# Performance work log

Hardware: AMD Instinct MI355X
Metric: run time of the kernel (lower is better)

Reference implementation:

```python
import jax, jax.numpy as jnp
import numpy as np

N_NODES = 100000
N_EDGES = 1600000
IN_CH = 128
NHIDDEN = 64
OUT_CH = 40
NLAYERS = 4
ALPHA = 0.1


def setup_inputs() -> dict:
    key = jax.random.key(0)
    ks = jax.random.split(key, 7)
    x = jax.random.normal(ks[0], (N_NODES, IN_CH), dtype=jnp.float32)
    edge_index = jax.random.randint(ks[1], (2, N_EDGES), 0, N_NODES, dtype=jnp.int64)
    batch_graph = jnp.zeros((N_NODES,), dtype=jnp.int64)
    fc1_w = jax.random.normal(ks[2], (NHIDDEN, IN_CH), dtype=jnp.float32) * (1.0 / np.sqrt(IN_CH))
    fc1_b = jax.random.normal(ks[3], (NHIDDEN,), dtype=jnp.float32) * 0.01
    conv_w = jax.random.normal(ks[4], (NLAYERS, NHIDDEN, NHIDDEN), dtype=jnp.float32) * (1.0 / np.sqrt(NHIDDEN))
    fc2_w = jax.random.normal(ks[5], (OUT_CH, NHIDDEN), dtype=jnp.float32) * (1.0 / np.sqrt(NHIDDEN))
    fc2_b = jax.random.normal(ks[6], (OUT_CH,), dtype=jnp.float32) * 0.01
    return {"x": x, "edge_index": edge_index, "batch_graph": batch_graph,
            "fc1_w": fc1_w, "fc1_b": fc1_b, "conv_w": conv_w,
            "fc2_w": fc2_w, "fc2_b": fc2_b}


def reference(x, edge_index, batch_graph, fc1_w, fc1_b, conv_w, fc2_w, fc2_b):
    # eval mode: dropout layers are identity
    n = x.shape[0]
    row, col = edge_index[0], edge_index[1]  # source, target

    # gcn_norm with add_self_loops=False: sym deg^-1/2 normalization
    deg = jax.ops.segment_sum(jnp.ones_like(row, dtype=x.dtype), col, num_segments=n)
    dinv = jnp.where(deg > 0, deg ** -0.5, 0.0)
    norm = (dinv[row] * dinv[col])[:, None]  # [E, 1]

    h = jax.nn.relu(x @ fc1_w.T + fc1_b)  # [N, nhidden]
    h0 = h
    nlayers = conv_w.shape[0]
    for i in range(nlayers):
        # GCN2Conv: aggregate, initial-residual mix, weight1 matmul (beta=1)
        agg = jax.ops.segment_sum(h[row] * norm, col, num_segments=n)
        mixed = (1.0 - ALPHA) * agg + ALPHA * h0
        h = jax.nn.relu(mixed @ conv_w[i])
    out = h @ fc2_w.T + fc2_b  # [N, out_channels]
    return out
```

## Files before the change

kernel.cpp:

```cpp
#include <hip/hip_runtime.h>
#include <hip/hip_fp16.h>

#define N_NODES 100000
#define N_EDGES 1600000
#define IN_CH   128
#define NHID    64
#define OUT_CH  40
#define NBLK    391
#define NBUCK   196
#define BCAP    8960
#define WECAP   256


__global__ __launch_bounds__(256) void k_scan1(const int* __restrict__ cnt,
                                               int* __restrict__ rowptr,
                                               int* __restrict__ bsum,
                                               float* __restrict__ dinv) {
    __shared__ int s[256];
    int t = threadIdx.x;
    int n = blockIdx.x * 256 + t;
    int v = (n < N_NODES) ? cnt[n] : 0;
    s[t] = v;
    __syncthreads();
    for (int off = 1; off < 256; off <<= 1) {
        int add = (t >= off) ? s[t - off] : 0;
        __syncthreads();
        s[t] += add;
        __syncthreads();
    }
    int incl = s[t];
    if (n < N_NODES) {
        rowptr[n] = incl - v;
        dinv[n] = (v > 0) ? rsqrtf((float)v) : 0.0f;
    }
    if (t == 255) bsum[blockIdx.x] = incl;
}

__global__ __launch_bounds__(512) void k_scan2(int* __restrict__ bsum) {
    __shared__ int s[512];
    int t = threadIdx.x;
    int v = (t < NBLK) ? bsum[t] : 0;
    s[t] = v;
    __syncthreads();
    for (int off = 1; off < 512; off <<= 1) {
        int add = (t >= off) ? s[t - off] : 0;
        __syncthreads();
        s[t] += add;
        __syncthreads();
    }
    if (t < NBLK) bsum[t] = s[t] - v;
}

__global__ __launch_bounds__(256) void k_scan3(const int* __restrict__ bsum,
                                               int* __restrict__ rowptr) {
    int n = blockIdx.x * 256 + threadIdx.x;
    if (n < N_NODES) rowptr[n] = rowptr[n] + bsum[n >> 8];
    if (blockIdx.x == 0 && threadIdx.x == 0) rowptr[N_NODES] = N_EDGES;
}


__global__ __launch_bounds__(256) void k_scatA(const int* __restrict__ ei,
                                               int* __restrict__ bucketCnt,
                                               int2* __restrict__ ebufA,
                                               int* __restrict__ cnt) {
    __shared__ int hist[NBUCK];
    __shared__ int base[NBUCK];
    int t = threadIdx.x;
    int chunk = blockIdx.x * 4096;
    for (int i = t; i < NBUCK; i += 256) hist[i] = 0;
    __syncthreads();
#pragma unroll 4
    for (int i = 0; i < 16; i++) {
        int e = chunk + i * 256 + t;
        if (e < N_EDGES) {
            int c = ei[N_EDGES + e];
            atomicAdd(&hist[c >> 9], 1);
            atomicAdd(&cnt[c], 1);
        }
    }
    __syncthreads();
    for (int b = t; b < NBUCK; b += 256) {
        int h = hist[b];
        base[b] = h ? atomicAdd(&bucketCnt[b], h) : 0;
    }
    __syncthreads();
#pragma unroll 4
    for (int i = 0; i < 16; i++) {
        int e = chunk + i * 256 + t;
        if (e < N_EDGES) {
            int r = ei[e], c = ei[N_EDGES + e];
            int pos = atomicAdd(&base[c >> 9], 1);
            ebufA[(size_t)(c >> 9) * BCAP + pos] = make_int2(r, c);
        }
    }
}


__global__ __launch_bounds__(256) void k_scatB(const int2* __restrict__ ebufA,
                                               const int* __restrict__ bucketCnt,
                                               const int* __restrict__ rowptr,
                                               int* __restrict__ e4) {
    __shared__ int lcur[512];
    int b = blockIdx.x;
    int nodeB = b * 512;
    int t = threadIdx.x;
    for (int i = t; i < 512; i += 256) {
        int node = nodeB + i;
        lcur[i] = (node < N_NODES) ? rowptr[node] : 0;
    }
    __syncthreads();
    int nE = bucketCnt[b];
    const int2* src = ebufA + (size_t)b * BCAP;
    for (int i = t; i < nE; i += 256) {
        int2 rc = src[i];
        int pos = atomicAdd(&lcur[rc.y - nodeB], 1);
        e4[pos] = rc.x;
    }
}

__device__ __forceinline__ void store_h4(__half* dst, float a, float b, float c, float d) {
    union { uint2 u; __half2 h[2]; } pk;
    pk.h[0] = __floats2half2_rn(a, b);
    pk.h[1] = __floats2half2_rn(c, d);
    *(uint2*)dst = pk.u;
}


__global__ __launch_bounds__(256, 4) void k_fc1(const float* __restrict__ x,
                                                const float* __restrict__ w,
                                                const float* __restrict__ b,
                                                const float* __restrict__ dinv,
                                                __half* __restrict__ h016,
                                                __half* __restrict__ hs1) {
    __shared__ float xs[64 * 128];
    int t = threadIdx.x;
    int nodeBase = blockIdx.x * 64;

    {
        int lane8 = t & 7, rhalf = t >> 3;
#pragma unroll
        for (int r2 = 0; r2 < 2; r2++) {
            int nl = r2 * 32 + rhalf;
            int n = nodeBase + nl;
            int swz = (nl ^ (nl >> 3)) & 7;
            float4* dstrow = (float4*)(xs + nl * 128);
            if (n < N_NODES) {
                const float4* src = (const float4*)(x + (size_t)n * IN_CH);
#pragma unroll
                for (int q = 0; q < 4; q++) dstrow[(q * 8 + lane8) ^ swz] = src[q * 8 + lane8];
            } else {
                float4 z = {0.f, 0.f, 0.f, 0.f};
#pragma unroll
                for (int q = 0; q < 4; q++) dstrow[(q * 8 + lane8) ^ swz] = z;
            }
        }
    }
    __syncthreads();

    int tx = t & 15, ty = t >> 4;
    int n0 = tx * 4, o0 = ty * 4;
    int swz0 = ((n0 + 0) ^ ((n0 + 0) >> 3)) & 7;
    int swz1 = ((n0 + 1) ^ ((n0 + 1) >> 3)) & 7;
    int swz2 = ((n0 + 2) ^ ((n0 + 2) >> 3)) & 7;
    int swz3 = ((n0 + 3) ^ ((n0 + 3) >> 3)) & 7;
    const float4* xrow0 = (const float4*)(xs + (n0 + 0) * 128);
    const float4* xrow1 = (const float4*)(xs + (n0 + 1) * 128);
    const float4* xrow2 = (const float4*)(xs + (n0 + 2) * 128);
    const float4* xrow3 = (const float4*)(xs + (n0 + 3) * 128);

    float c[4][4];
#pragma unroll
    for (int i = 0; i < 4; i++)
#pragma unroll
        for (int j = 0; j < 4; j++) c[i][j] = 0.f;

#pragma unroll 4
    for (int k = 0; k < IN_CH; k += 4) {
        int kk = k >> 2;
        float4 b0 = *(const float4*)&w[(size_t)(o0 + 0) * IN_CH + k];
        float4 b1 = *(const float4*)&w[(size_t)(o0 + 1) * IN_CH + k];
        float4 b2 = *(const float4*)&w[(size_t)(o0 + 2) * IN_CH + k];
        float4 b3 = *(const float4*)&w[(size_t)(o0 + 3) * IN_CH + k];
        float4 a0 = xrow0[kk ^ swz0];
        float4 a1 = xrow1[kk ^ swz1];
        float4 a2 = xrow2[kk ^ swz2];
        float4 a3 = xrow3[kk ^ swz3];
#pragma unroll
        for (int i = 0; i < 4; i++) {
            float4 a = (i == 0) ? a0 : (i == 1) ? a1 : (i == 2) ? a2 : a3;
            c[i][0] = fmaf(a.x, b0.x, fmaf(a.y, b0.y, fmaf(a.z, b0.z, fmaf(a.w, b0.w, c[i][0]))));
            c[i][1] = fmaf(a.x, b1.x, fmaf(a.y, b1.y, fmaf(a.z, b1.z, fmaf(a.w, b1.w, c[i][1]))));
            c[i][2] = fmaf(a.x, b2.x, fmaf(a.y, b2.y, fmaf(a.z, b2.z, fmaf(a.w, b2.w, c[i][2]))));
            c[i][3] = fmaf(a.x, b3.x, fmaf(a.y, b3.y, fmaf(a.z, b3.z, fmaf(a.w, b3.w, c[i][3]))));
        }
    }

    float4 bias = *(const float4*)&b[o0];
#pragma unroll
    for (int i = 0; i < 4; i++) {
        int n = nodeBase + n0 + i;
        if (n < N_NODES) {
            float vx = fmaxf(c[i][0] + bias.x, 0.f);
            float vy = fmaxf(c[i][1] + bias.y, 0.f);
            float vz = fmaxf(c[i][2] + bias.z, 0.f);
            float vw = fmaxf(c[i][3] + bias.w, 0.f);
            store_h4(&h016[(size_t)n * NHID + o0], vx, vy, vz, vw);
            float dn = dinv[n];
            store_h4(&hs1[(size_t)n * NHID + o0], vx * dn, vy * dn, vz * dn, vw * dn);
        }
    }
}


__global__ __launch_bounds__(256, 4) void k_conv(const __half* __restrict__ hs,
                                                 const __half* __restrict__ h0,
                                                 const int* __restrict__ rowptr,
                                                 const int* __restrict__ e4,
                                                 const float* __restrict__ W,
                                                 const float* __restrict__ dinv,
                                                 __half* __restrict__ hout,
                                                 int scaled) {
    __shared__ int   eSw[4][WECAP];
    __shared__ float mixs[4][8 * 68];
    int t = threadIdx.x;
    int wid = t >> 6, lane = t & 63;
    int wbase = blockIdx.x * 32 + wid * 8;
    int grp = lane >> 3;
    int cg = (lane & 7) * 8;
    int* eW = eSw[wid];
    float* mix = mixs[wid];

    int n = wbase + grp;
    int s = rowptr[n], e = rowptr[n + 1];
    int wb0 = rowptr[wbase];
    int wbN = rowptr[wbase + 8] - wb0;
    int nStage = (wbN < WECAP) ? wbN : WECAP;
    for (int i = lane; i < nStage; i += 64) eW[i] = e4[wb0 + i];

#define LOADM_G(pm, jb)                                                  \
    {                                                                    \
        _Pragma("unroll")                                                \
        for (int u = 0; u < 4; u++) {                                    \
            int idx = (jb) + u;                                          \
            pm[u] = (idx < e) ? e4[idx] : N_NODES;                       \
        }                                                                \
    }
#define LOADM(pm, jb)                                                    \
    {                                                                    \
        _Pragma("unroll")                                                \
        for (int u = 0; u < 4; u++) {                                    \
            int idx = (jb) + u;                                          \
            int m = N_NODES;                                             \
            if (idx < e) {                                               \
                int li = idx - wb0;                                      \
                m = (li < WECAP) ? eW[li] : e4[idx];                     \
            }                                                            \
            pm[u] = m;                                                   \
        }                                                                \
    }
#define ISSUE(pv, pm)                                                    \
    {                                                                    \
        _Pragma("unroll")                                                \
        for (int u = 0; u < 4; u++)                                      \
            pv[u] = *(const float4*)&hs[(size_t)pm[u] * NHID + cg];      \
    }
#define ACC4(cv)                                                         \
    {                                                                    \
        _Pragma("unroll")                                                \
        for (int u = 0; u < 4; u++) {                                    \
            const __half2* hp = (const __half2*)&cv[u];                  \
            _Pragma("unroll")                                            \
            for (int q = 0; q < 4; q++) {                                \
                float2 f = __half22float2(hp[q]);                       \
                acc[q * 2 + 0] += f.x;                                   \
                acc[q * 2 + 1] += f.y;                                   \
            }                                                            \
        }                                                                \
    }

    int    pmA[4], pmB[4];
    float4 pvA[4], pvB[4];
    LOADM_G(pmA, s);     ISSUE(pvA, pmA);
    LOADM_G(pmB, s + 4); ISSUE(pvB, pmB);

    float dn = dinv[n];
    float4 h0raw = *(const float4*)&h0[(size_t)n * NHID + cg];

    float acc[8];
#pragma unroll
    for (int i = 0; i < 8; i++) acc[i] = 0.f;

    __threadfence_block();

    for (int j = s; j < e; j += 8) {
        {
            float4 cv[4];
#pragma unroll
            for (int u = 0; u < 4; u++) cv[u] = pvA[u];
            int jn = j + 8;
            if (jn < e) { LOADM(pmA, jn); ISSUE(pvA, pmA); }
            ACC4(cv);
        }
        if (j + 4 < e) {
            float4 cv[4];
#pragma unroll
            for (int u = 0; u < 4; u++) cv[u] = pvB[u];
            int jn = j + 12;
            if (jn < e) { LOADM(pmB, jn); ISSUE(pvB, pmB); }
            ACC4(cv);
        }
    }
#undef LOADM_G
#undef LOADM
#undef ISSUE
#undef ACC4

    {
        const __half* h0h = (const __half*)&h0raw;
        float a = 0.9f * dn;
        float m[8];
#pragma unroll
        for (int q = 0; q < 8; q++)
            m[q] = fmaf(a, acc[q], 0.1f * __half2float(h0h[q]));
        float4 m0 = {m[0], m[1], m[2], m[3]};
        float4 m1 = {m[4], m[5], m[6], m[7]};
        *(float4*)&mix[grp * 68 + cg] = m0;
        *(float4*)&mix[grp * 68 + cg + 4] = m1;
    }
    __threadfence_block();

    int tx = lane & 15, ty = lane >> 4;
    int o0 = tx * 4, r0 = ty * 2;
    float c[2][4];
#pragma unroll
    for (int i = 0; i < 2; i++)
#pragma unroll
        for (int j = 0; j < 4; j++) c[i][j] = 0.f;

#pragma unroll 4
    for (int k = 0; k < NHID; k += 4) {
        float4 b0 = *(const float4*)&W[(k + 0) * NHID + o0];
        float4 b1 = *(const float4*)&W[(k + 1) * NHID + o0];
        float4 b2 = *(const float4*)&W[(k + 2) * NHID + o0];
        float4 b3 = *(const float4*)&W[(k + 3) * NHID + o0];
#pragma unroll
        for (int i = 0; i < 2; i++) {
            float4 a = *(const float4*)&mix[(r0 + i) * 68 + k];
            c[i][0] = fmaf(a.x, b0.x, fmaf(a.y, b1.x, fmaf(a.z, b2.x, fmaf(a.w, b3.x, c[i][0]))));
            c[i][1] = fmaf(a.x, b0.y, fmaf(a.y, b1.y, fmaf(a.z, b2.y, fmaf(a.w, b3.y, c[i][1]))));
            c[i][2] = fmaf(a.x, b0.z, fmaf(a.y, b1.z, fmaf(a.z, b2.z, fmaf(a.w, b3.z, c[i][2]))));
            c[i][3] = fmaf(a.x, b0.w, fmaf(a.y, b1.w, fmaf(a.z, b2.w, fmaf(a.w, b3.w, c[i][3]))));
        }
    }
#pragma unroll
    for (int i = 0; i < 2; i++) {
        int n2 = wbase + r0 + i;
        float sc = 1.0f;
        if (scaled) sc = dinv[n2];
        store_h4(&hout[(size_t)n2 * NHID + o0],
                 fmaxf(c[i][0], 0.f) * sc, fmaxf(c[i][1], 0.f) * sc,
                 fmaxf(c[i][2], 0.f) * sc, fmaxf(c[i][3], 0.f) * sc);
    }
}


__global__ __launch_bounds__(256) void k_fc2(const __half* __restrict__ h,
                                             const float* __restrict__ w,
                                             const float* __restrict__ b,
                                             float* __restrict__ out) {
    __shared__ float wT[NHID * 44];
    __shared__ float hsl[64 * 68];
    int t = threadIdx.x;
    int nodeBase = blockIdx.x * 64;

    for (int id = t; id < NHID * OUT_CH; id += 256) {
        int o = id >> 6, k = id & 63;
        wT[k * 44 + o] = w[id];
    }
    {
        int nl = t >> 2, seg = t & 3;
        int n = nodeBase + nl;
        float* dst = hsl + nl * 68 + seg * 16;
        if (n < N_NODES) {
            float4 raw0 = *(const float4*)&h[(size_t)n * NHID + seg * 16];
            float4 raw1 = *(const float4*)&h[(size_t)n * NHID + seg * 16 + 8];
            const __half2* hp0 = (const __half2*)&raw0;
            const __half2* hp1 = (const __half2*)&raw1;
#pragma unroll
            for (int q = 0; q < 4; q++) {
                float2 f = __half22float2(hp0[q]);
                dst[q * 2 + 0] = f.x;
                dst[q * 2 + 1] = f.y;
            }
#pragma unroll
            for (int q = 0; q < 4; q++) {
                float2 f = __half22float2(hp1[q]);
                dst[8 + q * 2 + 0] = f.x;
                dst[8 + q * 2 + 1] = f.y;
            }
        } else {
#pragma unroll
            for (int q = 0; q < 16; q++) dst[q] = 0.f;
        }
    }
    __syncthreads();

    if (t < 160) {
        int tx = t % 10, ty = t / 10;
        int o0 = tx * 4, n0 = ty * 4;
        float c[4][4];
#pragma unroll
        for (int i = 0; i < 4; i++)
#pragma unroll
            for (int j = 0; j < 4; j++) c[i][j] = 0.f;

#pragma unroll 4
        for (int k = 0; k < NHID; k += 4) {
            float4 b0 = *(const float4*)&wT[(k + 0) * 44 + o0];
            float4 b1 = *(const float4*)&wT[(k + 1) * 44 + o0];
            float4 b2 = *(const float4*)&wT[(k + 2) * 44 + o0];
            float4 b3 = *(const float4*)&wT[(k + 3) * 44 + o0];
#pragma unroll
            for (int i = 0; i < 4; i++) {
                float4 a = *(const float4*)&hsl[(n0 + i) * 68 + k];
                c[i][0] = fmaf(a.x, b0.x, fmaf(a.y, b1.x, fmaf(a.z, b2.x, fmaf(a.w, b3.x, c[i][0]))));
                c[i][1] = fmaf(a.x, b0.y, fmaf(a.y, b1.y, fmaf(a.z, b2.y, fmaf(a.w, b3.y, c[i][1]))));
                c[i][2] = fmaf(a.x, b0.z, fmaf(a.y, b1.z, fmaf(a.z, b2.z, fmaf(a.w, b3.z, c[i][2]))));
                c[i][3] = fmaf(a.x, b0.w, fmaf(a.y, b1.w, fmaf(a.z, b2.w, fmaf(a.w, b3.w, c[i][3]))));
            }
        }
        float4 bias = *(const float4*)&b[o0];
#pragma unroll
        for (int i = 0; i < 4; i++) {
            int n = nodeBase + n0 + i;
            if (n < N_NODES) {
                float4 v;
                v.x = c[i][0] + bias.x;
                v.y = c[i][1] + bias.y;
                v.z = c[i][2] + bias.z;
                v.w = c[i][3] + bias.w;
                *(float4*)&out[(size_t)n * OUT_CH + o0] = v;
            }
        }
    }
}


extern "C" void kernel_launch(void* const* d_in, const int* in_sizes, int n_in,
                              void* d_out, int out_size, void* d_ws, size_t ws_size,
                              hipStream_t stream) {
    const float* x    = (const float*)d_in[0];
    const int*   ei   = (const int*)d_in[1];
    const float* fc1w = (const float*)d_in[3];
    const float* fc1b = (const float*)d_in[4];
    const float* cw   = (const float*)d_in[5];
    const float* fc2w = (const float*)d_in[6];
    const float* fc2b = (const float*)d_in[7];
    float* out = (float*)d_out;

    char* p = (char*)d_ws;
    auto alloc = [&](size_t bytes) { char* r = p; p += (bytes + 255) & ~(size_t)255; return r; };
    __half* h016   = (__half*)alloc((size_t)N_NODES * NHID * 2);
    __half* hsA    = (__half*)alloc((size_t)(N_NODES + 1) * NHID * 2);
    __half* hsB    = (__half*)alloc((size_t)(N_NODES + 1) * NHID * 2);
    int*    e4     = (int*)   alloc((size_t)(N_EDGES + 8) * 4);
    int2*   ebufA  = (int2*)  alloc((size_t)NBUCK * BCAP * 8);
    int*    cnt    = (int*)   alloc((size_t)N_NODES * 4);
    int*    rowptr = (int*)   alloc((size_t)(N_NODES + 1) * 4);
    int*    bCnt   = (int*)   alloc((size_t)NBUCK * 4);
    float*  dinv   = (float*) alloc((size_t)N_NODES * 4);
    int*    bsum   = (int*)   alloc(512 * 4);
    __half* h4     = (__half*)ebufA;

    hipMemsetAsync(bCnt, 0, (size_t)NBUCK * 4, stream);
    hipMemsetAsync(cnt, 0, (size_t)N_NODES * 4, stream);
    hipMemsetAsync(hsA + (size_t)N_NODES * NHID, 0, NHID * 2, stream);
    hipMemsetAsync(hsB + (size_t)N_NODES * NHID, 0, NHID * 2, stream);

    k_scatA<<<(N_EDGES + 4095) / 4096, 256, 0, stream>>>(ei, bCnt, ebufA, cnt);
    k_scan1<<<NBLK, 256, 0, stream>>>(cnt, rowptr, bsum, dinv);
    k_scan2<<<1, 512, 0, stream>>>(bsum);
    k_scan3<<<NBLK, 256, 0, stream>>>(bsum, rowptr);
    k_scatB<<<NBUCK, 256, 0, stream>>>(ebufA, bCnt, rowptr, e4);

    int gb64 = (N_NODES + 63) / 64;
    int gb32 = N_NODES / 32;
    k_fc1 <<<gb64, 256, 0, stream>>>(x, fc1w, fc1b, dinv, h016, hsA);
    k_conv<<<gb32, 256, 0, stream>>>(hsA, h016, rowptr, e4, cw + 0 * NHID * NHID, dinv, hsB, 1);
    k_conv<<<gb32, 256, 0, stream>>>(hsB, h016, rowptr, e4, cw + 1 * NHID * NHID, dinv, hsA, 1);
    k_conv<<<gb32, 256, 0, stream>>>(hsA, h016, rowptr, e4, cw + 2 * NHID * NHID, dinv, hsB, 1);
    k_conv<<<gb32, 256, 0, stream>>>(hsB, h016, rowptr, e4, cw + 3 * NHID * NHID, dinv, h4, 0);
    k_fc2 <<<gb64, 256, 0, stream>>>(h4, fc2w, fc2b, out);
}
```

Measured before the change: 466.0 us.

## Pad CSR rows to multiples of eight, compute degrees per bucket, stage fc1 weights

Each node's CSR row is padded to a multiple of eight entries, with dummy neighbors pointing at a zero row, so the conv gather loop can drop its per-index bounds checks and the tail branch. Degree counting moves from global atomics in the edge scatter kernel to a separate per-bucket shared-memory histogram kernel, which also removes a memset. k_fc1 now stages the weight matrix in swizzled LDS and swaps the thread mapping. This costs a larger edge array, extra padding gathers, one more launch, and lower fc1 occupancy.

```diff
diff --git a/kernel.cpp b/kernel.cpp
--- a/kernel.cpp
+++ b/kernel.cpp
@@ -9,7 +9,8 @@
 #define NBLK    391
 #define NBUCK   196
 #define BCAP    8960
-#define WECAP   256
+#define WECAP   320
+#define E4CAP   (N_EDGES + 7 * N_NODES + 64)
 
 
 __global__ __launch_bounds__(256) void k_scan1(const int* __restrict__ cnt,
@@ -20,7 +21,8 @@
     int t = threadIdx.x;
     int n = blockIdx.x * 256 + t;
     int v = (n < N_NODES) ? cnt[n] : 0;
-    s[t] = v;
+    int pv = (v + 7) & ~7;
+    s[t] = pv;
     __syncthreads();
     for (int off = 1; off < 256; off <<= 1) {
         int add = (t >= off) ? s[t - off] : 0;
@@ -30,13 +32,14 @@
     }
     int incl = s[t];
     if (n < N_NODES) {
-        rowptr[n] = incl - v;
+        rowptr[n] = incl - pv;
         dinv[n] = (v > 0) ? rsqrtf((float)v) : 0.0f;
     }
     if (t == 255) bsum[blockIdx.x] = incl;
 }
 
-__global__ __launch_bounds__(512) void k_scan2(int* __restrict__ bsum) {
+__global__ __launch_bounds__(512) void k_scan2(int* __restrict__ bsum,
+                                               int* __restrict__ rowptr) {
     __shared__ int s[512];
     int t = threadIdx.x;
     int v = (t < NBLK) ? bsum[t] : 0;
@@ -48,6 +51,7 @@
         s[t] += add;
         __syncthreads();
     }
+    if (t == NBLK - 1) rowptr[N_NODES] = s[t];
     if (t < NBLK) bsum[t] = s[t] - v;
 }
 
@@ -55,14 +59,12 @@
                                                int* __restrict__ rowptr) {
     int n = blockIdx.x * 256 + threadIdx.x;
     if (n < N_NODES) rowptr[n] = rowptr[n] + bsum[n >> 8];
-    if (blockIdx.x == 0 && threadIdx.x == 0) rowptr[N_NODES] = N_EDGES;
 }
 
 
 __global__ __launch_bounds__(256) void k_scatA(const int* __restrict__ ei,
                                                int* __restrict__ bucketCnt,
-                                               int2* __restrict__ ebufA,
-                                               int* __restrict__ cnt) {
+                                               int2* __restrict__ ebufA) {
     __shared__ int hist[NBUCK];
     __shared__ int base[NBUCK];
     int t = threadIdx.x;
@@ -72,11 +74,7 @@
 #pragma unroll 4
     for (int i = 0; i < 16; i++) {
         int e = chunk + i * 256 + t;
-        if (e < N_EDGES) {
-            int c = ei[N_EDGES + e];
-            atomicAdd(&hist[c >> 9], 1);
-            atomicAdd(&cnt[c], 1);
-        }
+        if (e < N_EDGES) atomicAdd(&hist[ei[N_EDGES + e] >> 9], 1);
     }
     __syncthreads();
     for (int b = t; b < NBUCK; b += 256) {
@@ -96,6 +94,26 @@
 }
 
 
+__global__ __launch_bounds__(256) void k_deg(const int2* __restrict__ ebufA,
+                                             const int* __restrict__ bucketCnt,
+                                             int* __restrict__ cnt) {
+    __shared__ int hist[512];
+    int b = blockIdx.x;
+    int nodeB = b * 512;
+    int t = threadIdx.x;
+    for (int i = t; i < 512; i += 256) hist[i] = 0;
+    __syncthreads();
+    int nE = bucketCnt[b];
+    const int2* src = ebufA + (size_t)b * BCAP;
+    for (int i = t; i < nE; i += 256) atomicAdd(&hist[src[i].y - nodeB], 1);
+    __syncthreads();
+    for (int i = t; i < 512; i += 256) {
+        int node = nodeB + i;
+        if (node < N_NODES) cnt[node] = hist[i];
+    }
+}
+
+
 __global__ __launch_bounds__(256) void k_scatB(const int2* __restrict__ ebufA,
                                                const int* __restrict__ bucketCnt,
                                                const int* __restrict__ rowptr,
@@ -116,6 +134,14 @@
         int pos = atomicAdd(&lcur[rc.y - nodeB], 1);
         e4[pos] = rc.x;
     }
+    __syncthreads();
+    for (int i = t; i < 512; i += 256) {
+        int node = nodeB + i;
+        if (node < N_NODES) {
+            int end = rowptr[node + 1];
+            for (int pos = lcur[i]; pos < end; pos++) e4[pos] = N_NODES;
+        }
+    }
 }
 
 __device__ __forceinline__ void store_h4(__half* dst, float a, float b, float c, float d) {
@@ -126,13 +152,14 @@
 }
 
 
-__global__ __launch_bounds__(256, 4) void k_fc1(const float* __restrict__ x,
+__global__ __launch_bounds__(256, 2) void k_fc1(const float* __restrict__ x,
                                                 const float* __restrict__ w,
                                                 const float* __restrict__ b,
                                                 const float* __restrict__ dinv,
                                                 __half* __restrict__ h016,
                                                 __half* __restrict__ hs1) {
     __shared__ float xs[64 * 128];
+    __shared__ float wL[64 * 128];
     int t = threadIdx.x;
     int nodeBase = blockIdx.x * 64;
 
@@ -141,8 +168,8 @@
 #pragma unroll
         for (int r2 = 0; r2 < 2; r2++) {
             int nl = r2 * 32 + rhalf;
+            int swz = (nl ^ (nl >> 3)) & 7;
             int n = nodeBase + nl;
-            int swz = (nl ^ (nl >> 3)) & 7;
             float4* dstrow = (float4*)(xs + nl * 128);
             if (n < N_NODES) {
                 const float4* src = (const float4*)(x + (size_t)n * IN_CH);
@@ -153,20 +180,32 @@
 #pragma unroll
                 for (int q = 0; q < 4; q++) dstrow[(q * 8 + lane8) ^ swz] = z;
             }
+            float4* dstw = (float4*)(wL + nl * 128);
+            const float4* srcw = (const float4*)(w + (size_t)nl * IN_CH);
+#pragma unroll
+            for (int q = 0; q < 4; q++) dstw[(q * 8 + lane8) ^ swz] = srcw[q * 8 + lane8];
         }
     }
     __syncthreads();
 
     int tx = t & 15, ty = t >> 4;
-    int n0 = tx * 4, o0 = ty * 4;
-    int swz0 = ((n0 + 0) ^ ((n0 + 0) >> 3)) & 7;
-    int swz1 = ((n0 + 1) ^ ((n0 + 1) >> 3)) & 7;
-    int swz2 = ((n0 + 2) ^ ((n0 + 2) >> 3)) & 7;
-    int swz3 = ((n0 + 3) ^ ((n0 + 3) >> 3)) & 7;
-    const float4* xrow0 = (const float4*)(xs + (n0 + 0) * 128);
-    const float4* xrow1 = (const float4*)(xs + (n0 + 1) * 128);
-    const float4* xrow2 = (const float4*)(xs + (n0 + 2) * 128);
-    const float4* xrow3 = (const float4*)(xs + (n0 + 3) * 128);
+    int o0 = tx * 4, n0 = ty * 4;
+    int swzA0 = ((n0 + 0) ^ ((n0 + 0) >> 3)) & 7;
+    int swzA1 = ((n0 + 1) ^ ((n0 + 1) >> 3)) & 7;
+    int swzA2 = ((n0 + 2) ^ ((n0 + 2) >> 3)) & 7;
+    int swzA3 = ((n0 + 3) ^ ((n0 + 3) >> 3)) & 7;
+    int swzW0 = ((o0 + 0) ^ ((o0 + 0) >> 3)) & 7;
+    int swzW1 = ((o0 + 1) ^ ((o0 + 1) >> 3)) & 7;
+    int swzW2 = ((o0 + 2) ^ ((o0 + 2) >> 3)) & 7;
+    int swzW3 = ((o0 + 3) ^ ((o0 + 3) >> 3)) & 7;
+    const float4* ar0 = (const float4*)(xs + (n0 + 0) * 128);
+    const float4* ar1 = (const float4*)(xs + (n0 + 1) * 128);
+    const float4* ar2 = (const float4*)(xs + (n0 + 2) * 128);
+    const float4* ar3 = (const float4*)(xs + (n0 + 3) * 128);
+    const float4* wr0 = (const float4*)(wL + (o0 + 0) * 128);
+    const float4* wr1 = (const float4*)(wL + (o0 + 1) * 128);
+    const float4* wr2 = (const float4*)(wL + (o0 + 2) * 128);
+    const float4* wr3 = (const float4*)(wL + (o0 + 3) * 128);
 
     float c[4][4];
 #pragma unroll
@@ -177,14 +216,14 @@
 #pragma unroll 4
     for (int k = 0; k < IN_CH; k += 4) {
         int kk = k >> 2;
-        float4 b0 = *(const float4*)&w[(size_t)(o0 + 0) * IN_CH + k];
-        float4 b1 = *(const float4*)&w[(size_t)(o0 + 1) * IN_CH + k];
-        float4 b2 = *(const float4*)&w[(size_t)(o0 + 2) * IN_CH + k];
-        float4 b3 = *(const float4*)&w[(size_t)(o0 + 3) * IN_CH + k];
-        float4 a0 = xrow0[kk ^ swz0];
-        float4 a1 = xrow1[kk ^ swz1];
-        float4 a2 = xrow2[kk ^ swz2];
-        float4 a3 = xrow3[kk ^ swz3];
+        float4 b0 = wr0[kk ^ swzW0];
+        float4 b1 = wr1[kk ^ swzW1];
+        float4 b2 = wr2[kk ^ swzW2];
+        float4 b3 = wr3[kk ^ swzW3];
+        float4 a0 = ar0[kk ^ swzA0];
+        float4 a1 = ar1[kk ^ swzA1];
+        float4 a2 = ar2[kk ^ swzA2];
+        float4 a3 = ar3[kk ^ swzA3];
 #pragma unroll
         for (int i = 0; i < 4; i++) {
             float4 a = (i == 0) ? a0 : (i == 1) ? a1 : (i == 2) ? a2 : a3;
@@ -237,25 +276,13 @@
     int nStage = (wbN < WECAP) ? wbN : WECAP;
     for (int i = lane; i < nStage; i += 64) eW[i] = e4[wb0 + i];
 
-#define LOADM_G(pm, jb)                                                  \
-    {                                                                    \
-        _Pragma("unroll")                                                \
-        for (int u = 0; u < 4; u++) {                                    \
-            int idx = (jb) + u;                                          \
-            pm[u] = (idx < e) ? e4[idx] : N_NODES;                       \
-        }                                                                \
-    }
 #define LOADM(pm, jb)                                                    \
     {                                                                    \
         _Pragma("unroll")                                                \
         for (int u = 0; u < 4; u++) {                                    \
             int idx = (jb) + u;                                          \
-            int m = N_NODES;                                             \
-            if (idx < e) {                                               \
-                int li = idx - wb0;                                      \
-                m = (li < WECAP) ? eW[li] : e4[idx];                     \
-            }                                                            \
-            pm[u] = m;                                                   \
+            int li = idx - wb0;                                          \
+            pm[u] = (li < WECAP) ? eW[li] : e4[idx];                     \
         }                                                                \
     }
 #define ISSUE(pv, pm)                                                    \
@@ -271,7 +298,7 @@
             const __half2* hp = (const __half2*)&cv[u];                  \
             _Pragma("unroll")                                            \
             for (int q = 0; q < 4; q++) {                                \
-                float2 f = __half22float2(hp[q]);                       \
+                float2 f = __half22float2(hp[q]);                        \
                 acc[q * 2 + 0] += f.x;                                   \
                 acc[q * 2 + 1] += f.y;                                   \
             }                                                            \
@@ -280,8 +307,14 @@
 
     int    pmA[4], pmB[4];
     float4 pvA[4], pvB[4];
-    LOADM_G(pmA, s);     ISSUE(pvA, pmA);
-    LOADM_G(pmB, s + 4); ISSUE(pvB, pmB);
+    if (e > s) {
+#pragma unroll
+        for (int u = 0; u < 4; u++) pmA[u] = e4[s + u];
+        ISSUE(pvA, pmA);
+#pragma unroll
+        for (int u = 0; u < 4; u++) pmB[u] = e4[s + 4 + u];
+        ISSUE(pvB, pmB);
+    }
 
     float dn = dinv[n];
     float4 h0raw = *(const float4*)&h0[(size_t)n * NHID + cg];
@@ -301,7 +334,7 @@
             if (jn < e) { LOADM(pmA, jn); ISSUE(pvA, pmA); }
             ACC4(cv);
         }
-        if (j + 4 < e) {
+        {
             float4 cv[4];
 #pragma unroll
             for (int u = 0; u < 4; u++) cv[u] = pvB[u];
@@ -310,7 +343,6 @@
             ACC4(cv);
         }
     }
-#undef LOADM_G
 #undef LOADM
 #undef ISSUE
 #undef ACC4
@@ -463,7 +495,7 @@
     __half* h016   = (__half*)alloc((size_t)N_NODES * NHID * 2);
     __half* hsA    = (__half*)alloc((size_t)(N_NODES + 1) * NHID * 2);
     __half* hsB    = (__half*)alloc((size_t)(N_NODES + 1) * NHID * 2);
-    int*    e4     = (int*)   alloc((size_t)(N_EDGES + 8) * 4);
+    int*    e4     = (int*)   alloc((size_t)E4CAP * 4);
     int2*   ebufA  = (int2*)  alloc((size_t)NBUCK * BCAP * 8);
     int*    cnt    = (int*)   alloc((size_t)N_NODES * 4);
     int*    rowptr = (int*)   alloc((size_t)(N_NODES + 1) * 4);
@@ -473,13 +505,13 @@
     __half* h4     = (__half*)ebufA;
 
     hipMemsetAsync(bCnt, 0, (size_t)NBUCK * 4, stream);
-    hipMemsetAsync(cnt, 0, (size_t)N_NODES * 4, stream);
     hipMemsetAsync(hsA + (size_t)N_NODES * NHID, 0, NHID * 2, stream);
     hipMemsetAsync(hsB + (size_t)N_NODES * NHID, 0, NHID * 2, stream);
 
-    k_scatA<<<(N_EDGES + 4095) / 4096, 256, 0, stream>>>(ei, bCnt, ebufA, cnt);
+    k_scatA<<<(N_EDGES + 4095) / 4096, 256, 0, stream>>>(ei, bCnt, ebufA);
+    k_deg  <<<NBUCK, 256, 0, stream>>>(ebufA, bCnt, cnt);
     k_scan1<<<NBLK, 256, 0, stream>>>(cnt, rowptr, bsum, dinv);
-    k_scan2<<<1, 512, 0, stream>>>(bsum);
+    k_scan2<<<1, 512, 0, stream>>>(bsum, rowptr);
     k_scan3<<<NBLK, 256, 0, stream>>>(bsum, rowptr);
     k_scatB<<<NBUCK, 256, 0, stream>>>(ebufA, bCnt, rowptr, e4);
 
```

New measurement: 409.9 us. 1.14x faster.
